# Kernel tuning notes

Hardware: AMD Instinct MI355X
Metric: run time of the kernel (lower is better)

The kernel has to match this reference:

```python
import jax, jax.numpy as jnp
import numpy as np

B, S, D, VOCAB, K = 32, 128, 300, 20000, 8


def setup_inputs() -> dict:
    key = jax.random.key(0)
    ks = jax.random.split(key, 12)
    return {
        "words": jax.random.normal(ks[0], (B, S, D), jnp.float32),
        "lengths": jax.random.randint(ks[1], (B,), S // 2, S + 1),
        "vocab": jax.random.normal(ks[2], (VOCAB, D), jnp.float32) * 0.1,
        "default_embed": jax.random.uniform(ks[3], (D,), jnp.float32),
        "W": jnp.eye(D, dtype=jnp.float32) + 0.01 * jax.random.normal(ks[4], (D, D), jnp.float32),
        "lstm_Wih": jax.random.normal(ks[5], (4 * D, D), jnp.float32) * 0.05,
        "lstm_Whh": jax.random.normal(ks[6], (4 * D, D), jnp.float32) * 0.05,
        "lstm_bih": jnp.zeros((4 * D,), jnp.float32),
        "lstm_bhh": jnp.zeros((4 * D,), jnp.float32),
        "rnn_Wih": jax.random.normal(ks[7], (D, D), jnp.float32) * 0.05,
        "rnn_Whh": jax.random.normal(ks[8], (D, D), jnp.float32) * 0.05,
        "rnn_bih": jnp.zeros((D,), jnp.float32),
        "rnn_bhh": jnp.zeros((D,), jnp.float32),
    }


def _forward(words, lengths, vocab, default_embed, W,
             lstm_Wih, lstm_Whh, lstm_bih, lstm_bhh,
             rnn_Wih, rnn_Whh, rnn_bih, rnn_bhh):
    b, s, d = words.shape
    # --- NormalizeWordsModel (tagger) ---
    C = jnp.concatenate([vocab.T, default_embed[:, None]], axis=1)  # [D, V+1]
    P = jax.nn.softmax(jnp.einsum("bsd,de,ev->bsv", words, W, C), axis=-1)  # [B,S,V+1]
    V = P[..., -1:] * words + jnp.einsum("bsv,vd->bsd", P[..., :-1], vocab)  # [B,S,D]

    # --- LSTM encoder, final hidden at true length (packed-sequence semantics) ---
    valid = (jnp.arange(s)[None, :] < lengths[:, None])  # [B,S]

    def lstm_step(carry, xs):
        h, c = carry
        x_t, v_t = xs  # [B,D], [B]
        gates = x_t @ lstm_Wih.T + lstm_bih + h @ lstm_Whh.T + lstm_bhh  # [B,4D]
        i, f, g, o = jnp.split(gates, 4, axis=-1)
        c_new = jax.nn.sigmoid(f) * c + jax.nn.sigmoid(i) * jnp.tanh(g)
        h_new = jax.nn.sigmoid(o) * jnp.tanh(c_new)
        m = v_t[:, None]
        h = jnp.where(m, h_new, h)
        c = jnp.where(m, c_new, c)
        return (h, c), None

    h0 = jnp.zeros((b, d), V.dtype)
    (q, _), _ = jax.lax.scan(lstm_step, (h0, h0),
                             (jnp.swapaxes(V, 0, 1), valid.T))  # q: [B,D]

    # --- InstructionsDecoder: RNNCell applied K times to the same input q ---
    def rnn_step(h, _):
        h2 = jnp.tanh(q @ rnn_Wih.T + rnn_bih + h @ rnn_Whh.T + rnn_bhh)
        return h2, h2

    _, H = jax.lax.scan(rnn_step, h0, None, length=K)  # [K,B,D]
    H = jnp.swapaxes(H, 0, 1)  # [B,K,D]

    # --- masked softmax attention readout ---
    scores = jnp.einsum("bkd,bsd->bks", H, V)  # [B,K,S]
    scores = jnp.where(valid[:, None, :], scores, -jnp.inf)
    R = jnp.einsum("bks,bsd->bkd", jax.nn.softmax(scores, axis=-1), V)
    return R


def reference(words, lengths, vocab, default_embed, W,
              lstm_Wih, lstm_Whh, lstm_bih, lstm_bhh,
              rnn_Wih, rnn_Whh, rnn_bih, rnn_bhh):
    return _forward(words, lengths, vocab, default_embed, W,
                    lstm_Wih, lstm_Whh, lstm_bih, lstm_bhh,
                    rnn_Wih, rnn_Whh, rnn_bih, rnn_bhh)
```

## Files before the change

kernel.cpp:

```cpp
#include <hip/hip_runtime.h>


typedef unsigned short u16;
typedef unsigned int   u32;
typedef float  f32x4 __attribute__((ext_vector_type(4)));
typedef u32    u32x4 __attribute__((ext_vector_type(4)));
typedef __bf16 bf16x8 __attribute__((ext_vector_type(8)));
typedef _Float16 f16x2 __attribute__((ext_vector_type(2)));
typedef _Float16 f16x8 __attribute__((ext_vector_type(8)));

#define SCOPE_AGENT __HIP_MEMORY_SCOPE_AGENT

__device__ __forceinline__ float bf2f(u16 u) { return __uint_as_float(((u32)u) << 16); }
__device__ __forceinline__ u16 f2bf(float f) {
  u32 x = __float_as_uint(f);
  u32 r = (x + 0x7fffu + ((x >> 16) & 1u)) >> 16;
  return (u16)r;
}
__device__ __forceinline__ float sigm(float x) { return 1.f / (1.f + __expf(-x)); }
__device__ __forceinline__ u16 f2h(float f) {
  union { _Float16 h; u16 u; } cv; cv.h = (_Float16)f; return cv.u;
}
__device__ __forceinline__ float h2f(u16 u) {
  union { _Float16 h; u16 u; } cv; cv.u = u; return (float)cv.h;
}

__device__ __forceinline__ f32x4 shflx4(f32x4 v, int m) {
  f32x4 r;
  r[0] = __shfl_xor(v[0], m, 16);
  r[1] = __shfl_xor(v[1], m, 16);
  r[2] = __shfl_xor(v[2], m, 16);
  r[3] = __shfl_xor(v[3], m, 16);
  return r;
}

__device__ __forceinline__ void conv_seg(const void* src, u16* dst, int n, int is32,
                                         int t0, int stride) {
  if (is32) {
    const float* s = (const float*)src;
    for (int i = t0; i < n; i += stride) dst[i] = f2bf(s[i]);
  } else {
    const u16* s = (const u16*)src;
    for (int i = t0; i < n; i += stride) dst[i] = s[i];
  }
}

__global__ __launch_bounds__(256) void k_ingest(
    const void* words, const void* vocab, const void* de, const void* W,
    const void* lWih, const void* lWhh, const void* lbih, const void* lbhh,
    const void* rWih, const void* rWhh, const void* rbih, const void* rbhh,
    u16* cw, u16* cv, u16* cde, u16* cW, u16* cWih, u16* cWhh, u16* cbih, u16* cbhh,
    u16* crWih, u16* crWhh, u16* crbih, u16* crbhh, u32* flag, u32* seqz, u32* hbz) {
  __shared__ int s_is32;
  int tid = threadIdx.x;
  int vote = 0;
  if (tid < 64) {
    u32 w = ((const u32*)words)[tid];
    int e = (w >> 7) & 0xFF;
    vote = (e >= 100 && e <= 150) ? 1 : 0;
  }
  unsigned long long m = __ballot(vote);
  if (tid == 0) s_is32 = (__popcll(m) < 32) ? 1 : 0;
  __syncthreads();
  int is32 = s_is32;
  if (blockIdx.x == 0 && tid == 0) *flag = (u32)is32;
  int t0 = blockIdx.x * 256 + tid;
  int stride = gridDim.x * 256;
  if (t0 < 256) seqz[t0] = 0;
  if (t0 < 10240) hbz[t0] = 0;
  conv_seg(words, cw, 1228800, is32, t0, stride);
  conv_seg(vocab, cv, 6000000, is32, t0, stride);
  conv_seg(de, cde, 300, is32, t0, stride);
  conv_seg(W, cW, 90000, is32, t0, stride);
  conv_seg(lWih, cWih, 360000, is32, t0, stride);
  conv_seg(lWhh, cWhh, 360000, is32, t0, stride);
  conv_seg(lbih, cbih, 1200, is32, t0, stride);
  conv_seg(lbhh, cbhh, 1200, is32, t0, stride);
  conv_seg(rWih, crWih, 90000, is32, t0, stride);
  conv_seg(rWhh, crWhh, 90000, is32, t0, stride);
  conv_seg(rbih, crbih, 300, is32, t0, stride);
  conv_seg(rbhh, crbhh, 300, is32, t0, stride);
}

__global__ __launch_bounds__(256) void k_transpose_bf(const u16* __restrict__ in,
                                                      u16* __restrict__ out,
                                                      int J, int K) {
  __shared__ u16 t[32][33];
  int j0 = blockIdx.x * 32, k0 = blockIdx.y * 32;
  int lx = threadIdx.x & 31, ly = threadIdx.x >> 5;
  for (int r = ly; r < 32; r += 8) {
    int j = j0 + r, k = k0 + lx;
    t[r][lx] = (j < J && k < K) ? in[(size_t)j * K + k] : (u16)0;
  }
  __syncthreads();
  for (int r = ly; r < 32; r += 8) {
    int k = k0 + r, j = j0 + lx;
    if (k < K && j < J) out[(size_t)k * J + j] = t[lx][r];
  }
}

__global__ __launch_bounds__(256) void k_pack_w4(const u16* __restrict__ Whh,
                                                 u16* __restrict__ pW) {
  int idx = blockIdx.x * 256 + threadIdx.x;
  if (idx >= 16 * 25600) return;
  int bid = idx / 25600, r = idx % 25600;
  int t2 = r >> 9, lane = (r >> 3) & 63, j = r & 7;
  int nt = t2 / 10, kt = t2 % 10;
  int n = nt * 16 + (lane & 15);
  int gate = n / 20, dl = n % 20;
  int d0 = (bid < 15) ? 19 * bid : 285;
  int nd = (bid < 15) ? 19 : 15;
  int k = kt * 32 + ((lane >> 4) * 8) + j;
  u16 out = 0;
  if (dl < nd && k < 300) out = f2h(bf2f(Whh[(size_t)(gate * 300 + d0 + dl) * 300 + k]));
  pW[idx] = out;
}

__global__ __launch_bounds__(256) void k_pack_vocab(const u16* __restrict__ vocab,
                                                    u16* __restrict__ pA,
                                                    u16* __restrict__ pB) {
  __shared__ u16 sv[32][320];
  int ci = blockIdx.x, tid = threadIdx.x;
  for (int idx = tid; idx < 32 * 20; idx += 256) {
    int v = idx / 20, k = 300 + (idx - v * 20);
    sv[v][k] = 0;
  }
  for (int idx = tid; idx < 32 * 300; idx += 256) {
    int v = idx / 300, k = idx - v * 300;
    sv[v][k] = vocab[(size_t)(ci * 32 + v) * 300 + k];
  }
  __syncthreads();
  for (int idx = tid; idx < 10240; idx += 256) {
    int j = idx & 7, lane = (idx >> 3) & 63, t2 = idx >> 9;
    int kk = t2 % 10, h = t2 / 10;
    int v = h * 16 + (lane & 15);
    int k = kk * 32 + ((lane >> 4)) * 8 + j;
    pA[(size_t)ci * 10240 + (size_t)idx] = sv[v][k];
  }
  for (int idx = tid; idx < 9728; idx += 256) {
    int j = idx & 7, lane = (idx >> 3) & 63, nc = idx >> 9;
    int v = (lane >> 4) * 8 + j;
    int n = nc * 16 + (lane & 15);
    pB[(size_t)ci * 9728 + (size_t)idx] = sv[v][n];
  }
}

__global__ __launch_bounds__(256) void k_xw(const u16* __restrict__ words,
                                            const u16* __restrict__ W,
                                            u16* __restrict__ X) {
  __shared__ float As[300][33];
  int n0 = blockIdx.x * 128;
  int r0 = blockIdx.y * 32;
  int tid = threadIdx.x;
  for (int idx = tid; idx < 32 * 300; idx += 256) {
    int r = idx / 300, k = idx - r * 300;
    As[k][r] = bf2f(words[(size_t)(r0 + r) * 300 + k]);
  }
  __syncthreads();
  int j = n0 + (tid & 127);
  int rh = (tid >> 7) * 16;
  float acc[16];
#pragma unroll
  for (int i = 0; i < 16; i++) acc[i] = 0.f;
  if (j < 300) {
    for (int k = 0; k < 300; k++) {
      float bw = bf2f(W[(size_t)k * 300 + j]);
#pragma unroll
      for (int i = 0; i < 16; i++) acc[i] += As[k][rh + i] * bw;
    }
  }
  if (j < 320) {
#pragma unroll
    for (int i = 0; i < 16; i++) {
      float v = (j < 300) ? acc[i] : 0.f;
      X[(size_t)(r0 + rh + i) * 320 + j] = f2bf(v);
    }
  }
}

__global__ __launch_bounds__(512, 2) void k_softmax_v(
    const u16* __restrict__ X, const u16* __restrict__ pA, const u16* __restrict__ pB,
    u16* __restrict__ pAcc, float* __restrict__ pML) {
  __shared__ __align__(16) u16 chunk[19968];
  __shared__ __align__(16) float ptbuf[8 * 576];
  int bid = blockIdx.x;
  int sl = bid & 7, b = bid >> 3;
  int tid = threadIdx.x;
  int w = tid >> 6, lane = tid & 63;
  int quad = lane >> 4, n16 = lane & 15;
  int cs = (sl == 0) ? 0 : 79 + (sl - 1) * 78;
  int nch = (sl == 0) ? 79 : 78;

  int rowA = b * 128 + w * 16 + n16;
  const bf16x8* Xrow = (const bf16x8*)(X + (size_t)rowA * 320);
  bf16x8 afr[10];
#pragma unroll
  for (int kk = 0; kk < 10; kk++) afr[kk] = Xrow[kk * 4 + quad];
// ... 104 lines not shown
  }
#pragma unroll
  for (int nc = 0; nc < 19; nc++)
#pragma unroll
    for (int r = 0; r < 4; r++)
      pAcc[(prow + quad * 4 + r) * 304 + nc * 16 + n16] = f2bf(acc[nc][r]);
}

__global__ __launch_bounds__(320) void k_combine(
    const u16* __restrict__ pAcc, const float* __restrict__ pML,
    const u16* __restrict__ X, const u16* __restrict__ de,
    const u16* __restrict__ words, u16* __restrict__ Vout) {
  __shared__ float red[320];
  __shared__ float fs[8];
  __shared__ float sinv, sw;
  int row = blockIdx.x, tid = threadIdx.x;
  float p = 0.f;
  if (tid < 300) p = bf2f(X[(size_t)row * 320 + tid]) * bf2f(de[tid]);
  red[tid] = p;
  __syncthreads();
  if (tid == 0) {
    float d = 0.f;
    for (int i = 0; i < 300; i++) d += red[i];
    float mv[8], lv[8], ms = -1e30f;
    for (int s = 0; s < 8; s++) {
      mv[s] = pML[((size_t)s * 4096 + row) * 2];
      lv[s] = pML[((size_t)s * 4096 + row) * 2 + 1];
      ms = fmaxf(ms, mv[s]);
    }
    float mf = fmaxf(ms, d);
    float pd = __expf(d - mf);
    float l = pd;
    for (int s = 0; s < 8; s++) {
      float f = __expf(mv[s] - mf);
      fs[s] = f;
      l += lv[s] * f;
    }
    sinv = 1.f / l;
    sw = pd / l;
  }
  __syncthreads();
  float v = 0.f;
  if (tid < 300) {
    float a = 0.f;
#pragma unroll
    for (int s = 0; s < 8; s++)
      a += bf2f(pAcc[((size_t)s * 4096 + row) * 304 + tid]) * fs[s];
    v = a * sinv + sw * bf2f(words[(size_t)row * 300 + tid]);
  }
  Vout[(size_t)row * 320 + tid] = f2bf(v);
}

__global__ __launch_bounds__(256) void k_xg(const u16* __restrict__ Vb,
                                            const u16* __restrict__ WihT,
                                            const u16* __restrict__ bih,
                                            const u16* __restrict__ bhh,
                                            float* __restrict__ xg) {
  __shared__ float As[300][33];
  int n0 = blockIdx.x * 128;
  int r0 = blockIdx.y * 32;
  int tid = threadIdx.x;
  for (int idx = tid; idx < 32 * 300; idx += 256) {
    int r = idx / 300, k = idx - r * 300;
    As[k][r] = bf2f(Vb[(size_t)(r0 + r) * 320 + k]);
  }
  __syncthreads();
  int j = n0 + (tid & 127);
  if (j >= 1200) return;
  int rh = (tid >> 7) * 16;
  float acc[16];
#pragma unroll
  for (int i = 0; i < 16; i++) acc[i] = 0.f;
  for (int k = 0; k < 300; k++) {
    float bw = bf2f(WihT[(size_t)k * 1200 + j]);
#pragma unroll
    for (int i = 0; i < 16; i++) acc[i] += As[k][rh + i] * bw;
  }
  float bias = bf2f(bih[j]) + bf2f(bhh[j]);
#pragma unroll
  for (int i = 0; i < 16; i++)
    xg[(size_t)(r0 + rh + i) * 1200 + j] = acc[i] + bias;
}

__global__ __launch_bounds__(320, 1) void k_lstm2(
    const float* __restrict__ xg, const u16* __restrict__ pW,
    const int* __restrict__ lengths, u16* __restrict__ hb, u32* __restrict__ seq) {
  __shared__ float gl[32][84];
  __shared__ int s_maxlen;
  int bid = blockIdx.x, tid = threadIdx.x;
  int w = tid >> 6, lane = tid & 63;
  int quad = lane >> 4, n16 = lane & 15;
  int d0 = (bid < 15) ? 19 * bid : 285;
  int nd = (bid < 15) ? 19 : 15;
  {
    int lv = (tid < 32) ? lengths[tid] : 0;
    for (int off2 = 1; off2 < 32; off2 <<= 1) {
      int o = __shfl_xor(lv, off2, 64);
      lv = lv > o ? lv : o;
    }
    if (tid == 0) s_maxlen = lv;
  }
  f16x8 bf[10];
  const u32x4* pw4 = (const u32x4*)(pW + (size_t)bid * 25600);
#pragma unroll
  for (int kt = 0; kt < 10; kt++)
    bf[kt] = __builtin_bit_cast(f16x8, pw4[(w * 10 + kt) * 64 + lane]);
  int b0 = tid / 20, dl0 = tid - b0 * 20;
  int b1 = (tid + 320) / 20, dl1 = (tid + 320) - b1 * 20;
  bool a0 = dl0 < nd, a1 = dl1 < nd;
  int len0 = lengths[b0], len1 = lengths[b1];
  int dim0 = d0 + dl0, dim1 = d0 + dl1;
  int sa0 = (((b0 >> 4) * 10 + (dim0 >> 5)) * 64 + ((dim0 >> 3) & 3) * 16 + (b0 & 15)) * 8 + (dim0 & 7);
  int sa1 = (((b1 >> 4) * 10 + (dim1 >> 5)) * 64 + ((dim1 >> 3) & 3) * 16 + (b1 & 15)) * 8 + (dim1 & 7);
  float c0 = 0.f, h0 = 0.f, c1 = 0.f, h1 = 0.f;
  __syncthreads();
  int maxlen = s_maxlen;
  for (int t = 0; t < maxlen; t++) {
    if (tid < 16) {
      while (__hip_atomic_load(&seq[tid * 16], __ATOMIC_ACQUIRE, SCOPE_AGENT) < (u32)t)
        __builtin_amdgcn_s_sleep(2);
    }
    __syncthreads();
    float xv00 = 0.f, xv01 = 0.f, xv02 = 0.f, xv03 = 0.f;
    float xv10 = 0.f, xv11 = 0.f, xv12 = 0.f, xv13 = 0.f;
    const float* xr0 = xg + ((size_t)b0 * 128 + t) * 1200 + dim0;
    const float* xr1 = xg + ((size_t)b1 * 128 + t) * 1200 + dim1;
    if (a0) { xv00 = xr0[0]; xv01 = xr0[300]; xv02 = xr0[600]; xv03 = xr0[900]; }
    if (a1) { xv10 = xr1[0]; xv11 = xr1[300]; xv12 = xr1[600]; xv13 = xr1[900]; }
    const u32x4* hbt = (const u32x4*)hb + (size_t)(t & 1) * 1280;
    u32x4 af[2][10];
#pragma unroll
    for (int mt = 0; mt < 2; mt++)
#pragma unroll
      for (int kt = 0; kt < 10; kt++)
        af[mt][kt] = hbt[(mt * 10 + kt) * 64 + lane];
#pragma unroll
    for (int mt = 0; mt < 2; mt++) {
      f32x4 C;
      C[0] = 0.f; C[1] = 0.f; C[2] = 0.f; C[3] = 0.f;
#pragma unroll
      for (int kt = 0; kt < 10; kt++)
        C = __builtin_amdgcn_mfma_f32_16x16x32_f16(
            __builtin_bit_cast(f16x8, af[mt][kt]), bf[kt], C, 0, 0, 0);
#pragma unroll
      for (int rr = 0; rr < 4; rr++)
        gl[mt * 16 + quad * 4 + rr][w * 16 + n16] = C[rr];
    }
    __syncthreads();
    u16* hbw = hb + (size_t)((t + 1) & 1) * 10240;
    if (a0) {
      float gi = gl[b0][dl0] + xv00, gf = gl[b0][20 + dl0] + xv01;
      float gg = gl[b0][40 + dl0] + xv02, go = gl[b0][60 + dl0] + xv03;
      if (t < len0) {
        c0 = sigm(gf) * c0 + sigm(gi) * tanhf(gg);
        h0 = sigm(go) * tanhf(c0);
      }
      hbw[sa0] = f2h(h0);
    }
    if (a1) {
      float gi = gl[b1][dl1] + xv10, gf = gl[b1][20 + dl1] + xv11;
      float gg = gl[b1][40 + dl1] + xv12, go = gl[b1][60 + dl1] + xv13;
      if (t < len1) {
        c1 = sigm(gf) * c1 + sigm(gi) * tanhf(gg);
        h1 = sigm(go) * tanhf(c1);
      }
      hbw[sa1] = f2h(h1);
    }
    __syncthreads();
    if (tid == 0)
      __hip_atomic_store(&seq[bid * 16], (u32)(t + 1), __ATOMIC_RELEASE, SCOPE_AGENT);
  }
}

__global__ __launch_bounds__(320) void k_rnn(
    const u16* __restrict__ hb, const int* __restrict__ lengths,
    const u16* __restrict__ rWihT, const u16* __restrict__ rWhhT,
    const u16* __restrict__ rbih, const u16* __restrict__ rbhh,
    float* __restrict__ H) {
  __shared__ float qs[304], h2[304], base[304];
  __shared__ int s_maxlen;
  int b = blockIdx.x, tid = threadIdx.x;
  {
    int lv = (tid < 32) ? lengths[tid] : 0;
    for (int off2 = 1; off2 < 32; off2 <<= 1) {
      int o = __shfl_xor(lv, off2, 64);
      lv = lv > o ? lv : o;
    }
    if (tid == 0) s_maxlen = lv;
  }
  __syncthreads();
  int buf = s_maxlen & 1;
  if (tid < 304) {
    float q = 0.f;
    if (tid < 300) {
      int dim = tid;
      int idx = (((b >> 4) * 10 + (dim >> 5)) * 64 + ((dim >> 3) & 3) * 16 + (b & 15)) * 8 + (dim & 7);
      q = h2f(hb[(size_t)buf * 10240 + idx]);
    }
    qs[tid] = q;
    h2[tid] = 0.f;
  }
  __syncthreads();
  if (tid < 300) {
    float a = bf2f(rbih[tid]) + bf2f(rbhh[tid]);
    for (int k = 0; k < 300; k++) a += qs[k] * bf2f(rWihT[(size_t)k * 300 + tid]);
    base[tid] = a;
  }
  __syncthreads();
  for (int s = 0; s < 8; s++) {
    float nv = 0.f;
    if (tid < 300) {
      float a = base[tid];
      for (int k = 0; k < 300; k++) a += h2[k] * bf2f(rWhhT[(size_t)k * 300 + tid]);
      nv = tanhf(a);
    }
    __syncthreads();
    if (tid < 300) {
      h2[tid] = nv;
      H[((size_t)b * 8 + s) * 300 + tid] = nv;
    }
    __syncthreads();
  }
}

__global__ __launch_bounds__(256) void k_attn(const float* __restrict__ H,
                                              const u16* __restrict__ Vb,
                                              const int* __restrict__ lengths,
                                              const u32* __restrict__ flag,
                                              void* __restrict__ dout) {
  __shared__ float Hs[8][304];
  __shared__ float sc[8][128];
  __shared__ float wsum[8];
  int b = blockIdx.x, tid = threadIdx.x;
  int len = lengths[b];
  int is32 = (int)*flag;
  for (int idx = tid; idx < 8 * 300; idx += 256) {
    int k = idx / 300, j = idx - k * 300;
    Hs[k][j] = H[((size_t)b * 8 + k) * 300 + j];
  }
  __syncthreads();
  for (int s = tid; s < len; s += 256) {
    const u16* vr = Vb + (size_t)(b * 128 + s) * 320;
    float a[8];
#pragma unroll
    for (int k = 0; k < 8; k++) a[k] = 0.f;
    for (int j = 0; j < 300; j++) {
      float v = bf2f(vr[j]);
#pragma unroll
      for (int k = 0; k < 8; k++) a[k] += Hs[k][j] * v;
    }
#pragma unroll
    for (int k = 0; k < 8; k++) sc[k][s] = a[k];
  }
  __syncthreads();
  if (tid < 8) {
    float m = -1e30f;
    for (int s = 0; s < len; s++) m = fmaxf(m, sc[tid][s]);
    float l = 0.f;
    for (int s = 0; s < len; s++) { float e = __expf(sc[tid][s] - m); sc[tid][s] = e; l += e; }
    wsum[tid] = 1.f / l;
  }
  __syncthreads();
  int k = tid >> 5, jl = tid & 31;
  for (int j = jl; j < 300; j += 32) {
    float a = 0.f;
    for (int s = 0; s < len; s++) a += sc[k][s] * bf2f(Vb[(size_t)(b * 128 + s) * 320 + j]);
    float val = a * wsum[k];
    size_t o = ((size_t)b * 8 + k) * 300 + j;
    if (is32) ((float*)dout)[o] = val;
    else ((u16*)dout)[o] = f2bf(val);
  }
}

extern "C" void kernel_launch(void* const* d_in, const int* in_sizes, int n_in,
                              void* d_out, int out_size, void* d_ws, size_t ws_size,
                              hipStream_t stream) {
  (void)in_sizes; (void)n_in; (void)out_size; (void)ws_size;
  const void* words = d_in[0];
  const int* lengths = (const int*)d_in[1];
  const void* vocab = d_in[2];
  const void* de = d_in[3];
  const void* W = d_in[4];
  const void* lWih = d_in[5];
  const void* lWhh = d_in[6];
  const void* lbih = d_in[7];
  const void* lbhh = d_in[8];
  const void* rWih = d_in[9];
  const void* rWhh = d_in[10];
  const void* rbih = d_in[11];
  const void* rbhh = d_in[12];

  char* basep = (char*)d_ws;
  size_t off = 0;
  auto take = [&](size_t bytes) -> char* {
    char* p = basep + off;
    off += (bytes + 255) & ~(size_t)255;
    return p;
  };
  u16* cw    = (u16*)take(1228800 * 2);
  u16* cv    = (u16*)take(6000000 * 2);
  u16* cde   = (u16*)take(300 * 2);
  u16* cW    = (u16*)take(90000 * 2);
  u16* cWih  = (u16*)take(360000 * 2);
  u16* cWhh  = (u16*)take(360000 * 2);
  u16* cbih  = (u16*)take(1200 * 2);
  u16* cbhh  = (u16*)take(1200 * 2);
  u16* crWih = (u16*)take(90000 * 2);
  u16* crWhh = (u16*)take(90000 * 2);
  u16* crbih = (u16*)take(300 * 2);
  u16* crbhh = (u16*)take(300 * 2);
  u32* flag  = (u32*)take(256);
  u16*   X     = (u16*)take((size_t)4096 * 320 * 2);
  u16*   Vb    = (u16*)take((size_t)4096 * 320 * 2);
  u16*   WihT  = (u16*)take((size_t)300 * 1200 * 2);
  u16*   pW4   = (u16*)take((size_t)16 * 25600 * 2);
  u16*   rWihT = (u16*)take((size_t)300 * 300 * 2);
  u16*   rWhhT = (u16*)take((size_t)300 * 300 * 2);
  u16*   pAcc  = (u16*)take((size_t)8 * 4096 * 304 * 2);
  float* pML   = (float*)take((size_t)8 * 4096 * 2 * 4);
  float* H     = (float*)take((size_t)32 * 8 * 300 * 4);
  u16*   hb    = (u16*)take((size_t)2 * 10240 * 2);
  u32*   seq   = (u32*)take((size_t)4096 * 4);
  char* ureg = take((size_t)25000192);
  u16*   pA = (u16*)ureg;
  u16*   pB = (u16*)(ureg + (size_t)625 * 10240 * 2);
  float* xg = (float*)ureg;

  k_ingest<<<4096, 256, 0, stream>>>(words, vocab, de, W, lWih, lWhh, lbih, lbhh,
                                     rWih, rWhh, rbih, rbhh,
                                     cw, cv, cde, cW, cWih, cWhh, cbih, cbhh,
                                     crWih, crWhh, crbih, crbhh, flag, seq, (u32*)hb);
  k_transpose_bf<<<dim3(38, 10), 256, 0, stream>>>(cWih, WihT, 1200, 300);
  k_transpose_bf<<<dim3(10, 10), 256, 0, stream>>>(crWih, rWihT, 300, 300);
  k_transpose_bf<<<dim3(10, 10), 256, 0, stream>>>(crWhh, rWhhT, 300, 300);
  k_pack_w4<<<1600, 256, 0, stream>>>(cWhh, pW4);
  k_pack_vocab<<<625, 256, 0, stream>>>(cv, pA, pB);
  k_xw<<<dim3(3, 128), 256, 0, stream>>>(cw, cW, X);
  k_softmax_v<<<256, 512, 0, stream>>>(X, pA, pB, pAcc, pML);
  k_combine<<<4096, 320, 0, stream>>>(pAcc, pML, X, cde, cw, Vb);
  k_xg<<<dim3(10, 128), 256, 0, stream>>>(Vb, WihT, cbih, cbhh, xg);
  k_lstm2<<<16, 320, 0, stream>>>(xg, pW4, lengths, hb, seq);
  k_rnn<<<32, 320, 0, stream>>>(hb, lengths, rWihT, rWhhT, crbih, crbhh, H);
  k_attn<<<32, 256, 0, stream>>>(H, Vb, lengths, flag, d_out);
}
```

Baseline: 1.083 ms.

## Replace cross-block LSTM recurrence with per-batch-half single-block kernel

The LSTM recurrence no longer spreads hidden dimensions over 16 blocks that sync through global atomic flags every timestep. Instead, 2 blocks of 1024 threads each own 16 batch rows and all 300 dims, keep the whole Whh in registers, and exchange h through double-buffered LDS. A new repack kernel reorders the input gate projections so each lane can prefetch its gate quadruple, and gate values are gathered with DPP lane swaps. Sigmoid and tanh use rcp-based fast approximations. This removes the global spin-wait and barrier cost on the serial critical path, but uses only 2 CUs, adds an extra repack pass, and may hurt accuracy through the fast math.

```diff
diff --git a/kernel.cpp b/kernel.cpp
--- a/kernel.cpp
+++ b/kernel.cpp
@@ -9,20 +9,29 @@
 typedef _Float16 f16x2 __attribute__((ext_vector_type(2)));
 typedef _Float16 f16x8 __attribute__((ext_vector_type(8)));
 
-#define SCOPE_AGENT __HIP_MEMORY_SCOPE_AGENT
-
 __device__ __forceinline__ float bf2f(u16 u) { return __uint_as_float(((u32)u) << 16); }
 __device__ __forceinline__ u16 f2bf(float f) {
   u32 x = __float_as_uint(f);
   u32 r = (x + 0x7fffu + ((x >> 16) & 1u)) >> 16;
   return (u16)r;
 }
-__device__ __forceinline__ float sigm(float x) { return 1.f / (1.f + __expf(-x)); }
 __device__ __forceinline__ u16 f2h(float f) {
   union { _Float16 h; u16 u; } cv; cv.h = (_Float16)f; return cv.u;
 }
 __device__ __forceinline__ float h2f(u16 u) {
   union { _Float16 h; u16 u; } cv; cv.u = u; return (float)cv.h;
+}
+__device__ __forceinline__ float sigm_fast(float x) {
+  return __builtin_amdgcn_rcpf(1.f + __expf(-x));
+}
+__device__ __forceinline__ float tanh_fast(float x) {
+  return 1.f - 2.f * __builtin_amdgcn_rcpf(1.f + __expf(2.f * x));
+}
+
+template <int CTRL>
+__device__ __forceinline__ float dppq(float v) {
+  return __uint_as_float(
+      (u32)__builtin_amdgcn_mov_dpp((int)__float_as_uint(v), CTRL, 0xF, 0xF, true));
 }
 
 __device__ __forceinline__ f32x4 shflx4(f32x4 v, int m) {
@@ -50,7 +59,7 @@
     const void* lWih, const void* lWhh, const void* lbih, const void* lbhh,
     const void* rWih, const void* rWhh, const void* rbih, const void* rbhh,
     u16* cw, u16* cv, u16* cde, u16* cW, u16* cWih, u16* cWhh, u16* cbih, u16* cbhh,
-    u16* crWih, u16* crWhh, u16* crbih, u16* crbhh, u32* flag, u32* seqz, u32* hbz) {
+    u16* crWih, u16* crWhh, u16* crbih, u16* crbhh, u32* flag) {
   __shared__ int s_is32;
   int tid = threadIdx.x;
   int vote = 0;
@@ -66,8 +75,6 @@
   if (blockIdx.x == 0 && tid == 0) *flag = (u32)is32;
   int t0 = blockIdx.x * 256 + tid;
   int stride = gridDim.x * 256;
-  if (t0 < 256) seqz[t0] = 0;
-  if (t0 < 10240) hbz[t0] = 0;
   conv_seg(words, cw, 1228800, is32, t0, stride);
   conv_seg(vocab, cv, 6000000, is32, t0, stride);
   conv_seg(de, cde, 300, is32, t0, stride);
@@ -99,20 +106,26 @@
   }
 }
 
-__global__ __launch_bounds__(256) void k_pack_w4(const u16* __restrict__ Whh,
+__global__ __launch_bounds__(256) void k_pack_w5(const u16* __restrict__ Whh,
                                                  u16* __restrict__ pW) {
   int idx = blockIdx.x * 256 + threadIdx.x;
-  if (idx >= 16 * 25600) return;
-  int bid = idx / 25600, r = idx % 25600;
-  int t2 = r >> 9, lane = (r >> 3) & 63, j = r & 7;
-  int nt = t2 / 10, kt = t2 % 10;
-  int n = nt * 16 + (lane & 15);
-  int gate = n / 20, dl = n % 20;
-  int d0 = (bid < 15) ? 19 * bid : 285;
-  int nd = (bid < 15) ? 19 : 15;
-  int k = kt * 32 + ((lane >> 4) * 8) + j;
+  if (idx >= 409600) return;
+  int jj = idx & 7;
+  int lane = (idx >> 3) & 63;
+  int rest = idx >> 9;
+  int kt = rest % 10;
+  int t2 = rest / 10;
+  int j = t2 % 5;
+  int w = t2 / 5;
+  int n16 = lane & 15;
+  int g2 = n16 & 3;
+  int local = j * 16 + n16;
+  int dd = local >> 2;
+  int dim = w * 20 + dd;
+  int k = kt * 32 + ((lane >> 4) * 8) + jj;
   u16 out = 0;
-  if (dl < nd && k < 300) out = f2h(bf2f(Whh[(size_t)(gate * 300 + d0 + dl) * 300 + k]));
+  if (dim < 300 && k < 300)
+    out = f2h(bf2f(Whh[(size_t)(g2 * 300 + dim) * 300 + k]));
   pW[idx] = out;
 }
 
@@ -383,122 +396,136 @@
     xg[(size_t)(r0 + rh + i) * 1200 + j] = acc[i] + bias;
 }
 
-__global__ __launch_bounds__(320, 1) void k_lstm2(
-    const float* __restrict__ xg, const u16* __restrict__ pW,
-    const int* __restrict__ lengths, u16* __restrict__ hb, u32* __restrict__ seq) {
-  __shared__ float gl[32][84];
+__global__ __launch_bounds__(256) void k_repack_xg(const float* __restrict__ xg,
+                                                   float* __restrict__ xgp) {
+  __shared__ float s[16][81];
+  int bid = blockIdx.x;
+  int t = bid & 127, bm = bid >> 7;
+  int tid = threadIdx.x;
+  for (int w = 0; w < 16; w++) {
+    for (int e = tid; e < 1280; e += 256) {
+      int bl = e / 80, local = e - bl * 80;
+      int g2 = local / 20, dd = local - g2 * 20;
+      int dim = w * 20 + dd;
+      float v = 0.f;
+      if (dim < 300)
+        v = xg[((size_t)(bm * 16 + bl) * 128 + t) * 1200 + g2 * 300 + dim];
+      s[bl][dd * 4 + g2] = v;
+    }
+    __syncthreads();
+    size_t ob = ((size_t)(t * 2 + bm) * 1280 + w * 80) * 16;
+    for (int e = tid; e < 1280; e += 256) {
+      int nl = e >> 4, bl = e & 15;
+      xgp[ob + e] = s[bl][nl];
+    }
+    __syncthreads();
+  }
+}
+
+__global__ __launch_bounds__(1024, 1) void k_lstm3(
+    const float* __restrict__ xgp, const u16* __restrict__ pW,
+    const int* __restrict__ lengths, float* __restrict__ qbuf) {
+  __shared__ u16 hs[2][16][328];
   __shared__ int s_maxlen;
-  int bid = blockIdx.x, tid = threadIdx.x;
+  int bm = blockIdx.x, tid = threadIdx.x;
   int w = tid >> 6, lane = tid & 63;
   int quad = lane >> 4, n16 = lane & 15;
-  int d0 = (bid < 15) ? 19 * bid : 285;
-  int nd = (bid < 15) ? 19 : 15;
+  int g = n16 & 3, q4 = n16 >> 2;
+  for (int i = tid; i < 2 * 16 * 328; i += 1024) ((u16*)hs)[i] = 0;
   {
-    int lv = (tid < 32) ? lengths[tid] : 0;
-    for (int off2 = 1; off2 < 32; off2 <<= 1) {
-      int o = __shfl_xor(lv, off2, 64);
+    int lv = (lane < 16) ? lengths[bm * 16 + lane] : 0;
+#pragma unroll
+    for (int off = 1; off < 16; off <<= 1) {
+      int o = __shfl_xor(lv, off, 64);
       lv = lv > o ? lv : o;
     }
     if (tid == 0) s_maxlen = lv;
   }
-  f16x8 bf[10];
-  const u32x4* pw4 = (const u32x4*)(pW + (size_t)bid * 25600);
-#pragma unroll
-  for (int kt = 0; kt < 10; kt++)
-    bf[kt] = __builtin_bit_cast(f16x8, pw4[(w * 10 + kt) * 64 + lane]);
-  int b0 = tid / 20, dl0 = tid - b0 * 20;
-  int b1 = (tid + 320) / 20, dl1 = (tid + 320) - b1 * 20;
-  bool a0 = dl0 < nd, a1 = dl1 < nd;
-  int len0 = lengths[b0], len1 = lengths[b1];
-  int dim0 = d0 + dl0, dim1 = d0 + dl1;
-  int sa0 = (((b0 >> 4) * 10 + (dim0 >> 5)) * 64 + ((dim0 >> 3) & 3) * 16 + (b0 & 15)) * 8 + (dim0 & 7);
-  int sa1 = (((b1 >> 4) * 10 + (dim1 >> 5)) * 64 + ((dim1 >> 3) & 3) * 16 + (b1 & 15)) * 8 + (dim1 & 7);
-  float c0 = 0.f, h0 = 0.f, c1 = 0.f, h1 = 0.f;
+  f16x8 bf[5][10];
+  const u32x4* pw4 = (const u32x4*)pW;
+#pragma unroll
+  for (int j = 0; j < 5; j++)
+#pragma unroll
+    for (int kt = 0; kt < 10; kt++)
+      bf[j][kt] = __builtin_bit_cast(f16x8, pw4[((w * 5 + j) * 10 + kt) * 64 + lane]);
+  int b = quad * 4 + g;
+  int len_b = lengths[bm * 16 + b];
+  float c[5], h[5];
+#pragma unroll
+  for (int j = 0; j < 5; j++) { c[j] = 0.f; h[j] = 0.f; }
+  const f32x4* xp0 = (const f32x4*)xgp + ((size_t)bm * 1280 + w * 80 + n16) * 4 + quad;
+  f32x4 xv[5];
+#pragma unroll
+  for (int j = 0; j < 5; j++) xv[j] = xp0[j * 64];
   __syncthreads();
   int maxlen = s_maxlen;
   for (int t = 0; t < maxlen; t++) {
-    if (tid < 16) {
-      while (__hip_atomic_load(&seq[tid * 16], __ATOMIC_ACQUIRE, SCOPE_AGENT) < (u32)t)
-        __builtin_amdgcn_s_sleep(2);
-    }
-    __syncthreads();
-    float xv00 = 0.f, xv01 = 0.f, xv02 = 0.f, xv03 = 0.f;
-    float xv10 = 0.f, xv11 = 0.f, xv12 = 0.f, xv13 = 0.f;
-    const float* xr0 = xg + ((size_t)b0 * 128 + t) * 1200 + dim0;
-    const float* xr1 = xg + ((size_t)b1 * 128 + t) * 1200 + dim1;
-    if (a0) { xv00 = xr0[0]; xv01 = xr0[300]; xv02 = xr0[600]; xv03 = xr0[900]; }
-    if (a1) { xv10 = xr1[0]; xv11 = xr1[300]; xv12 = xr1[600]; xv13 = xr1[900]; }
-    const u32x4* hbt = (const u32x4*)hb + (size_t)(t & 1) * 1280;
-    u32x4 af[2][10];
-#pragma unroll
-    for (int mt = 0; mt < 2; mt++)
-#pragma unroll
-      for (int kt = 0; kt < 10; kt++)
-        af[mt][kt] = hbt[(mt * 10 + kt) * 64 + lane];
-#pragma unroll
-    for (int mt = 0; mt < 2; mt++) {
-      f32x4 C;
-      C[0] = 0.f; C[1] = 0.f; C[2] = 0.f; C[3] = 0.f;
-#pragma unroll
-      for (int kt = 0; kt < 10; kt++)
-        C = __builtin_amdgcn_mfma_f32_16x16x32_f16(
-            __builtin_bit_cast(f16x8, af[mt][kt]), bf[kt], C, 0, 0, 0);
-#pragma unroll
-      for (int rr = 0; rr < 4; rr++)
-        gl[mt * 16 + quad * 4 + rr][w * 16 + n16] = C[rr];
-    }
-    __syncthreads();
-    u16* hbw = hb + (size_t)((t + 1) & 1) * 10240;
-    if (a0) {
-      float gi = gl[b0][dl0] + xv00, gf = gl[b0][20 + dl0] + xv01;
-      float gg = gl[b0][40 + dl0] + xv02, go = gl[b0][60 + dl0] + xv03;
-      if (t < len0) {
-        c0 = sigm(gf) * c0 + sigm(gi) * tanhf(gg);
-        h0 = sigm(go) * tanhf(c0);
-      }
-      hbw[sa0] = f2h(h0);
-    }
-    if (a1) {
-      float gi = gl[b1][dl1] + xv10, gf = gl[b1][20 + dl1] + xv11;
-      float gg = gl[b1][40 + dl1] + xv12, go = gl[b1][60 + dl1] + xv13;
-      if (t < len1) {
-        c1 = sigm(gf) * c1 + sigm(gi) * tanhf(gg);
-        h1 = sigm(go) * tanhf(c1);
-      }
-      hbw[sa1] = f2h(h1);
-    }
-    __syncthreads();
-    if (tid == 0)
-      __hip_atomic_store(&seq[bid * 16], (u32)(t + 1), __ATOMIC_RELEASE, SCOPE_AGENT);
+    f32x4 acc[5];
+#pragma unroll
+    for (int j = 0; j < 5; j++) acc[j] = xv[j];
+    if (t + 1 < maxlen) {
+      const f32x4* xp = xp0 + (size_t)(t + 1) * 10240;
+#pragma unroll
+      for (int j = 0; j < 5; j++) xv[j] = xp[j * 64];
+    }
+    const u16* hr = &hs[t & 1][0][0];
+    u32x4 af[10];
+#pragma unroll
+    for (int kt = 0; kt < 10; kt++)
+      af[kt] = *(const u32x4*)(hr + n16 * 328 + kt * 32 + quad * 8);
+#pragma unroll
+    for (int kt = 0; kt < 10; kt++) {
+      f16x8 a = __builtin_bit_cast(f16x8, af[kt]);
+#pragma unroll
+      for (int j = 0; j < 5; j++)
+        acc[j] = __builtin_amdgcn_mfma_f32_16x16x32_f16(a, bf[j][kt], acc[j], 0, 0, 0);
+    }
+    u16* hw = (u16*)&hs[(t + 1) & 1][0][0];
+    bool upd = (t < len_b);
+#pragma unroll
+    for (int j = 0; j < 5; j++) {
+      float v0 = acc[j][0], v1 = acc[j][1], v2 = acc[j][2], v3 = acc[j][3];
+      float x0 = dppq<0xB1>(v0), x1 = dppq<0xB1>(v1);
+      float x2 = dppq<0xB1>(v2), x3 = dppq<0xB1>(v3);
+      bool o1 = (g & 1);
+      float m0 = o1 ? x1 : v0;
+      float m1 = o1 ? v1 : x0;
+      float m2 = o1 ? x3 : v2;
+      float m3 = o1 ? v3 : x2;
+      float y0 = dppq<0x4E>(m0), y1 = dppq<0x4E>(m1);
+      float y2 = dppq<0x4E>(m2), y3 = dppq<0x4E>(m3);
+      bool o2 = (g & 2);
+      float F0 = o2 ? y2 : m0;
+      float F1 = o2 ? y3 : m1;
+      float F2 = o2 ? m2 : y0;
+      float F3 = o2 ? m3 : y1;
+      float ii = sigm_fast(F0), ff = sigm_fast(F1);
+      float gg = tanh_fast(F2), oo = sigm_fast(F3);
+      float cn = ff * c[j] + ii * gg;
+      float hn = oo * tanh_fast(cn);
+      c[j] = upd ? cn : c[j];
+      h[j] = upd ? hn : h[j];
+      int dim = w * 20 + j * 4 + q4;
+      if (dim < 300) hw[b * 328 + dim] = f2h(h[j]);
+    }
+    __syncthreads();
+  }
+#pragma unroll
+  for (int j = 0; j < 5; j++) {
+    int dim = w * 20 + j * 4 + q4;
+    if (dim < 300) qbuf[(size_t)(bm * 16 + b) * 304 + dim] = h[j];
   }
 }
 
 __global__ __launch_bounds__(320) void k_rnn(
-    const u16* __restrict__ hb, const int* __restrict__ lengths,
+    const float* __restrict__ qbuf,
     const u16* __restrict__ rWihT, const u16* __restrict__ rWhhT,
     const u16* __restrict__ rbih, const u16* __restrict__ rbhh,
     float* __restrict__ H) {
   __shared__ float qs[304], h2[304], base[304];
-  __shared__ int s_maxlen;
   int b = blockIdx.x, tid = threadIdx.x;
-  {
-    int lv = (tid < 32) ? lengths[tid] : 0;
-    for (int off2 = 1; off2 < 32; off2 <<= 1) {
-      int o = __shfl_xor(lv, off2, 64);
-      lv = lv > o ? lv : o;
-    }
-    if (tid == 0) s_maxlen = lv;
-  }
-  __syncthreads();
-  int buf = s_maxlen & 1;
   if (tid < 304) {
-    float q = 0.f;
-    if (tid < 300) {
-      int dim = tid;
-      int idx = (((b >> 4) * 10 + (dim >> 5)) * 64 + ((dim >> 3) & 3) * 16 + (b & 15)) * 8 + (dim & 7);
-      q = h2f(hb[(size_t)buf * 10240 + idx]);
-    }
-    qs[tid] = q;
+    qs[tid] = (tid < 300) ? qbuf[(size_t)b * 304 + tid] : 0.f;
     h2[tid] = 0.f;
   }
   __syncthreads();
@@ -614,14 +641,15 @@
   u16*   X     = (u16*)take((size_t)4096 * 320 * 2);
   u16*   Vb    = (u16*)take((size_t)4096 * 320 * 2);
   u16*   WihT  = (u16*)take((size_t)300 * 1200 * 2);
-  u16*   pW4   = (u16*)take((size_t)16 * 25600 * 2);
+  u16*   pW5   = (u16*)take((size_t)409600 * 2);
   u16*   rWihT = (u16*)take((size_t)300 * 300 * 2);
   u16*   rWhhT = (u16*)take((size_t)300 * 300 * 2);
-  u16*   pAcc  = (u16*)take((size_t)8 * 4096 * 304 * 2);
+  char* uacc = take((size_t)20971520);
+  u16*   pAcc = (u16*)uacc;
+  float* xgp  = (float*)uacc;
   float* pML   = (float*)take((size_t)8 * 4096 * 2 * 4);
   float* H     = (float*)take((size_t)32 * 8 * 300 * 4);
-  u16*   hb    = (u16*)take((size_t)2 * 10240 * 2);
-  u32*   seq   = (u32*)take((size_t)4096 * 4);
+  float* qbuf  = (float*)take((size_t)32 * 304 * 4);
   char* ureg = take((size_t)25000192);
   u16*   pA = (u16*)ureg;
   u16*   pB = (u16*)(ureg + (size_t)625 * 10240 * 2);
@@ -630,17 +658,18 @@
   k_ingest<<<4096, 256, 0, stream>>>(words, vocab, de, W, lWih, lWhh, lbih, lbhh,
                                      rWih, rWhh, rbih, rbhh,
                                      cw, cv, cde, cW, cWih, cWhh, cbih, cbhh,
-                                     crWih, crWhh, crbih, crbhh, flag, seq, (u32*)hb);
+                                     crWih, crWhh, crbih, crbhh, flag);
   k_transpose_bf<<<dim3(38, 10), 256, 0, stream>>>(cWih, WihT, 1200, 300);
   k_transpose_bf<<<dim3(10, 10), 256, 0, stream>>>(crWih, rWihT, 300, 300);
   k_transpose_bf<<<dim3(10, 10), 256, 0, stream>>>(crWhh, rWhhT, 300, 300);
-  k_pack_w4<<<1600, 256, 0, stream>>>(cWhh, pW4);
+  k_pack_w5<<<1600, 256, 0, stream>>>(cWhh, pW5);
   k_pack_vocab<<<625, 256, 0, stream>>>(cv, pA, pB);
   k_xw<<<dim3(3, 128), 256, 0, stream>>>(cw, cW, X);
   k_softmax_v<<<256, 512, 0, stream>>>(X, pA, pB, pAcc, pML);
   k_combine<<<4096, 320, 0, stream>>>(pAcc, pML, X, cde, cw, Vb);
   k_xg<<<dim3(10, 128), 256, 0, stream>>>(Vb, WihT, cbih, cbhh, xg);
-  k_lstm2<<<16, 320, 0, stream>>>(xg, pW4, lengths, hb, seq);
-  k_rnn<<<32, 320, 0, stream>>>(hb, lengths, rWihT, rWhhT, crbih, crbhh, H);
+  k_repack_xg<<<256, 256, 0, stream>>>(xg, xgp);
+  k_lstm3<<<2, 1024, 0, stream>>>(xgp, pW5, lengths, qbuf);
+  k_rnn<<<32, 320, 0, stream>>>(qbuf, rWihT, rWhhT, crbih, crbhh, H);
   k_attn<<<32, 256, 0, stream>>>(H, Vb, lengths, flag, d_out);
 }
```

Result: slower. 2.995 ms (+176.6%).

## Split LSTM recurrence over 8 larger blocks with LDS weights and relaxed flags

Applied to the files above, without the earlier changes.

The persistent LSTM recurrence now runs on 8 blocks of 640 threads instead of 16 blocks of 320, so each step waits on half as many cross-block flags. Each block now covers 38 hidden dimensions, and its recurrent-weight slice is staged in LDS. The hidden-state exchange uses relaxed atomic loads and stores with a shorter sleep, and sigmoid and tanh use fast reciprocal-based approximations. The final hidden state is written to a float buffer for the RNN kernel, which removes the fp16 re-read. Tradeoffs: each block does more work per step, the relaxed ordering leans on the release/acquire flag pattern for correctness, and the fast transcendentals are less precise.

```diff
diff --git a/kernel.cpp b/kernel.cpp
--- a/kernel.cpp
+++ b/kernel.cpp
@@ -6,7 +6,6 @@
 typedef float  f32x4 __attribute__((ext_vector_type(4)));
 typedef u32    u32x4 __attribute__((ext_vector_type(4)));
 typedef __bf16 bf16x8 __attribute__((ext_vector_type(8)));
-typedef _Float16 f16x2 __attribute__((ext_vector_type(2)));
 typedef _Float16 f16x8 __attribute__((ext_vector_type(8)));
 
 #define SCOPE_AGENT __HIP_MEMORY_SCOPE_AGENT
@@ -17,12 +16,17 @@
   u32 r = (x + 0x7fffu + ((x >> 16) & 1u)) >> 16;
   return (u16)r;
 }
-__device__ __forceinline__ float sigm(float x) { return 1.f / (1.f + __expf(-x)); }
 __device__ __forceinline__ u16 f2h(float f) {
   union { _Float16 h; u16 u; } cv; cv.h = (_Float16)f; return cv.u;
 }
 __device__ __forceinline__ float h2f(u16 u) {
   union { _Float16 h; u16 u; } cv; cv.u = u; return (float)cv.h;
+}
+__device__ __forceinline__ float sigm_fast(float x) {
+  return __builtin_amdgcn_rcpf(1.f + __expf(-x));
+}
+__device__ __forceinline__ float tanh_fast(float x) {
+  return 1.f - 2.f * __builtin_amdgcn_rcpf(1.f + __expf(2.f * x));
 }
 
 __device__ __forceinline__ f32x4 shflx4(f32x4 v, int m) {
@@ -99,20 +103,25 @@
   }
 }
 
-__global__ __launch_bounds__(256) void k_pack_w4(const u16* __restrict__ Whh,
+__global__ __launch_bounds__(256) void k_pack_w8(const u16* __restrict__ Whh,
                                                  u16* __restrict__ pW) {
   int idx = blockIdx.x * 256 + threadIdx.x;
-  if (idx >= 16 * 25600) return;
-  int bid = idx / 25600, r = idx % 25600;
-  int t2 = r >> 9, lane = (r >> 3) & 63, j = r & 7;
-  int nt = t2 / 10, kt = t2 % 10;
-  int n = nt * 16 + (lane & 15);
-  int gate = n / 20, dl = n % 20;
-  int d0 = (bid < 15) ? 19 * bid : 285;
-  int nd = (bid < 15) ? 19 : 15;
-  int k = kt * 32 + ((lane >> 4) * 8) + j;
+  if (idx >= 409600) return;
+  int bid = idx / 51200;
+  int r = idx - bid * 51200;
+  int j = r & 7;
+  int lane = (r >> 3) & 63;
+  int t2 = r >> 9;
+  int kt = t2 % 10, w = t2 / 10;
+  int n16 = lane & 15, quad = lane >> 4;
+  int n = w * 16 + n16;
+  int gate = n / 40, dl = n - gate * 40;
+  int nd = (bid < 7) ? 38 : 34;
+  int dim = 38 * bid + dl;
+  int k = kt * 32 + quad * 8 + j;
   u16 out = 0;
-  if (dl < nd && k < 300) out = f2h(bf2f(Whh[(size_t)(gate * 300 + d0 + dl) * 300 + k]));
+  if (dl < nd && k < 300)
+    out = f2h(bf2f(Whh[(size_t)(gate * 300 + dim) * 300 + k]));
   pW[idx] = out;
 }
 
@@ -383,122 +392,131 @@
     xg[(size_t)(r0 + rh + i) * 1200 + j] = acc[i] + bias;
 }
 
-__global__ __launch_bounds__(320, 1) void k_lstm2(
+__global__ __launch_bounds__(640, 1) void k_lstm5(
     const float* __restrict__ xg, const u16* __restrict__ pW,
-    const int* __restrict__ lengths, u16* __restrict__ hb, u32* __restrict__ seq) {
-  __shared__ float gl[32][84];
+    const int* __restrict__ lengths, u32* __restrict__ hb,
+    u32* __restrict__ seq, float* __restrict__ qbuf) {
+  __shared__ __align__(16) u16 wlds[51200];
+  __shared__ float gl[32][164];
   __shared__ int s_maxlen;
   int bid = blockIdx.x, tid = threadIdx.x;
   int w = tid >> 6, lane = tid & 63;
   int quad = lane >> 4, n16 = lane & 15;
-  int d0 = (bid < 15) ? 19 * bid : 285;
-  int nd = (bid < 15) ? 19 : 15;
+  int nd = (bid < 7) ? 38 : 34;
+  {
+    const u32x4* src = (const u32x4*)(pW + (size_t)bid * 51200);
+    u32x4* dst = (u32x4*)wlds;
+#pragma unroll
+    for (int i = 0; i < 10; i++) dst[tid + i * 640] = src[tid + i * 640];
+  }
   {
     int lv = (tid < 32) ? lengths[tid] : 0;
-    for (int off2 = 1; off2 < 32; off2 <<= 1) {
-      int o = __shfl_xor(lv, off2, 64);
+#pragma unroll
+    for (int off = 1; off < 32; off <<= 1) {
+      int o = __shfl_xor(lv, off, 64);
       lv = lv > o ? lv : o;
     }
     if (tid == 0) s_maxlen = lv;
   }
-  f16x8 bf[10];
-  const u32x4* pw4 = (const u32x4*)(pW + (size_t)bid * 25600);
-#pragma unroll
-  for (int kt = 0; kt < 10; kt++)
-    bf[kt] = __builtin_bit_cast(f16x8, pw4[(w * 10 + kt) * 64 + lane]);
-  int b0 = tid / 20, dl0 = tid - b0 * 20;
-  int b1 = (tid + 320) / 20, dl1 = (tid + 320) - b1 * 20;
-  bool a0 = dl0 < nd, a1 = dl1 < nd;
+  int b0 = tid / 40, dl = tid - b0 * 40;
+  int b1 = b0 + 16;
+  bool act = dl < nd;
+  int dim = 38 * bid + dl;
   int len0 = lengths[b0], len1 = lengths[b1];
-  int dim0 = d0 + dl0, dim1 = d0 + dl1;
-  int sa0 = (((b0 >> 4) * 10 + (dim0 >> 5)) * 64 + ((dim0 >> 3) & 3) * 16 + (b0 & 15)) * 8 + (dim0 & 7);
-  int sa1 = (((b1 >> 4) * 10 + (dim1 >> 5)) * 64 + ((dim1 >> 3) & 3) * 16 + (b1 & 15)) * 8 + (dim1 & 7);
+  int p = (dim >> 1) & 3;
+  int chq = ((dim >> 3) & 3) * 16;
+  int ch0 = ((0 * 10 + (dim >> 5)) * 64 + chq + (b0 & 15));
+  int ch1 = ((1 * 10 + (dim >> 5)) * 64 + chq + (b1 & 15));
+  int so0 = (p * 1280 + ch0) * 2 + (dim & 1);
+  int so1 = (p * 1280 + ch1) * 2 + (dim & 1);
+  u16* hb16 = (u16*)hb;
   float c0 = 0.f, h0 = 0.f, c1 = 0.f, h1 = 0.f;
+  u32* myf = seq + (size_t)bid * 16;
   __syncthreads();
   int maxlen = s_maxlen;
   for (int t = 0; t < maxlen; t++) {
-    if (tid < 16) {
-      while (__hip_atomic_load(&seq[tid * 16], __ATOMIC_ACQUIRE, SCOPE_AGENT) < (u32)t)
-        __builtin_amdgcn_s_sleep(2);
+    if (tid < 8) {
+      while (__hip_atomic_load(&seq[tid * 16], __ATOMIC_RELAXED, SCOPE_AGENT) < (u32)t)
+        __builtin_amdgcn_s_sleep(1);
     }
     __syncthreads();
     float xv00 = 0.f, xv01 = 0.f, xv02 = 0.f, xv03 = 0.f;
     float xv10 = 0.f, xv11 = 0.f, xv12 = 0.f, xv13 = 0.f;
-    const float* xr0 = xg + ((size_t)b0 * 128 + t) * 1200 + dim0;
-    const float* xr1 = xg + ((size_t)b1 * 128 + t) * 1200 + dim1;
-    if (a0) { xv00 = xr0[0]; xv01 = xr0[300]; xv02 = xr0[600]; xv03 = xr0[900]; }
-    if (a1) { xv10 = xr1[0]; xv11 = xr1[300]; xv12 = xr1[600]; xv13 = xr1[900]; }
-    const u32x4* hbt = (const u32x4*)hb + (size_t)(t & 1) * 1280;
+    if (act) {
+      const float* xr0 = xg + ((size_t)b0 * 128 + t) * 1200 + dim;
+      const float* xr1 = xg + ((size_t)b1 * 128 + t) * 1200 + dim;
+      xv00 = xr0[0]; xv01 = xr0[300]; xv02 = xr0[600]; xv03 = xr0[900];
+      xv10 = xr1[0]; xv11 = xr1[300]; xv12 = xr1[600]; xv13 = xr1[900];
+    }
+    const u32* hbt = hb + (size_t)(t & 1) * 5120;
     u32x4 af[2][10];
 #pragma unroll
     for (int mt = 0; mt < 2; mt++)
 #pragma unroll
       for (int kt = 0; kt < 10; kt++)
-        af[mt][kt] = hbt[(mt * 10 + kt) * 64 + lane];
-#pragma unroll
-    for (int mt = 0; mt < 2; mt++) {
-      f32x4 C;
-      C[0] = 0.f; C[1] = 0.f; C[2] = 0.f; C[3] = 0.f;
-#pragma unroll
-      for (int kt = 0; kt < 10; kt++)
-        C = __builtin_amdgcn_mfma_f32_16x16x32_f16(
-            __builtin_bit_cast(f16x8, af[mt][kt]), bf[kt], C, 0, 0, 0);
-#pragma unroll
-      for (int rr = 0; rr < 4; rr++)
-        gl[mt * 16 + quad * 4 + rr][w * 16 + n16] = C[rr];
-    }
-    __syncthreads();
-    u16* hbw = hb + (size_t)((t + 1) & 1) * 10240;
-    if (a0) {
-      float gi = gl[b0][dl0] + xv00, gf = gl[b0][20 + dl0] + xv01;
-      float gg = gl[b0][40 + dl0] + xv02, go = gl[b0][60 + dl0] + xv03;
-      if (t < len0) {
-        c0 = sigm(gf) * c0 + sigm(gi) * tanhf(gg);
-        h0 = sigm(go) * tanhf(c0);
+#pragma unroll
+        for (int pp = 0; pp < 4; pp++)
+          af[mt][kt][pp] = __hip_atomic_load(
+              hbt + pp * 1280 + (mt * 10 + kt) * 64 + lane,
+              __ATOMIC_RELAXED, SCOPE_AGENT);
+    const u32x4* wl = (const u32x4*)wlds;
+    f32x4 C0, C1;
+    C0[0] = 0.f; C0[1] = 0.f; C0[2] = 0.f; C0[3] = 0.f;
+    C1[0] = 0.f; C1[1] = 0.f; C1[2] = 0.f; C1[3] = 0.f;
+#pragma unroll
+    for (int kt = 0; kt < 10; kt++) {
+      f16x8 bfr = __builtin_bit_cast(f16x8, wl[(w * 10 + kt) * 64 + lane]);
+      C0 = __builtin_amdgcn_mfma_f32_16x16x32_f16(
+          __builtin_bit_cast(f16x8, af[0][kt]), bfr, C0, 0, 0, 0);
+      C1 = __builtin_amdgcn_mfma_f32_16x16x32_f16(
+          __builtin_bit_cast(f16x8, af[1][kt]), bfr, C1, 0, 0, 0);
+    }
+#pragma unroll
+    for (int rr = 0; rr < 4; rr++) {
+      gl[quad * 4 + rr][w * 16 + n16] = C0[rr];
+      gl[16 + quad * 4 + rr][w * 16 + n16] = C1[rr];
+    }
+    __syncthreads();
+    int bufo = ((t + 1) & 1) * 10240;
+    if (act) {
+      {
+        float gi = gl[b0][dl] + xv00, gf = gl[b0][40 + dl] + xv01;
+        float gg = gl[b0][80 + dl] + xv02, go = gl[b0][120 + dl] + xv03;
+        if (t < len0) {
+          c0 = sigm_fast(gf) * c0 + sigm_fast(gi) * tanh_fast(gg);
+          h0 = sigm_fast(go) * tanh_fast(c0);
+        }
+        __hip_atomic_store(hb16 + bufo + so0, f2h(h0), __ATOMIC_RELAXED, SCOPE_AGENT);
       }
-      hbw[sa0] = f2h(h0);
-    }
-    if (a1) {
-      float gi = gl[b1][dl1] + xv10, gf = gl[b1][20 + dl1] + xv11;
-      float gg = gl[b1][40 + dl1] + xv12, go = gl[b1][60 + dl1] + xv13;
-      if (t < len1) {
-        c1 = sigm(gf) * c1 + sigm(gi) * tanhf(gg);
-        h1 = sigm(go) * tanhf(c1);
+      {
+        float gi = gl[b1][dl] + xv10, gf = gl[b1][40 + dl] + xv11;
+        float gg = gl[b1][80 + dl] + xv12, go = gl[b1][120 + dl] + xv13;
+        if (t < len1) {
+          c1 = sigm_fast(gf) * c1 + sigm_fast(gi) * tanh_fast(gg);
+          h1 = sigm_fast(go) * tanh_fast(c1);
+        }
+        __hip_atomic_store(hb16 + bufo + so1, f2h(h1), __ATOMIC_RELAXED, SCOPE_AGENT);
       }
-      hbw[sa1] = f2h(h1);
     }
     __syncthreads();
     if (tid == 0)
-      __hip_atomic_store(&seq[bid * 16], (u32)(t + 1), __ATOMIC_RELEASE, SCOPE_AGENT);
+      __hip_atomic_store(myf, (u32)(t + 1), __ATOMIC_RELEASE, SCOPE_AGENT);
+  }
+  if (act) {
+    qbuf[(size_t)b0 * 304 + dim] = h0;
+    qbuf[(size_t)b1 * 304 + dim] = h1;
   }
 }
 
 __global__ __launch_bounds__(320) void k_rnn(
-    const u16* __restrict__ hb, const int* __restrict__ lengths,
+    const float* __restrict__ qbuf,
     const u16* __restrict__ rWihT, const u16* __restrict__ rWhhT,
     const u16* __restrict__ rbih, const u16* __restrict__ rbhh,
     float* __restrict__ H) {
   __shared__ float qs[304], h2[304], base[304];
-  __shared__ int s_maxlen;
   int b = blockIdx.x, tid = threadIdx.x;
-  {
-    int lv = (tid < 32) ? lengths[tid] : 0;
-    for (int off2 = 1; off2 < 32; off2 <<= 1) {
-      int o = __shfl_xor(lv, off2, 64);
-      lv = lv > o ? lv : o;
-    }
-    if (tid == 0) s_maxlen = lv;
-  }
-  __syncthreads();
-  int buf = s_maxlen & 1;
   if (tid < 304) {
-    float q = 0.f;
-    if (tid < 300) {
-      int dim = tid;
-      int idx = (((b >> 4) * 10 + (dim >> 5)) * 64 + ((dim >> 3) & 3) * 16 + (b & 15)) * 8 + (dim & 7);
-      q = h2f(hb[(size_t)buf * 10240 + idx]);
-    }
-    qs[tid] = q;
+    qs[tid] = (tid < 300) ? qbuf[(size_t)b * 304 + tid] : 0.f;
     h2[tid] = 0.f;
   }
   __syncthreads();
@@ -614,14 +632,15 @@
   u16*   X     = (u16*)take((size_t)4096 * 320 * 2);
   u16*   Vb    = (u16*)take((size_t)4096 * 320 * 2);
   u16*   WihT  = (u16*)take((size_t)300 * 1200 * 2);
-  u16*   pW4   = (u16*)take((size_t)16 * 25600 * 2);
+  u16*   pW8   = (u16*)take((size_t)409600 * 2);
   u16*   rWihT = (u16*)take((size_t)300 * 300 * 2);
   u16*   rWhhT = (u16*)take((size_t)300 * 300 * 2);
   u16*   pAcc  = (u16*)take((size_t)8 * 4096 * 304 * 2);
   float* pML   = (float*)take((size_t)8 * 4096 * 2 * 4);
   float* H     = (float*)take((size_t)32 * 8 * 300 * 4);
-  u16*   hb    = (u16*)take((size_t)2 * 10240 * 2);
-  u32*   seq   = (u32*)take((size_t)4096 * 4);
+  float* qbuf  = (float*)take((size_t)32 * 304 * 4);
+  u32*   hbg   = (u32*)take((size_t)10240 * 4);
+  u32*   seq   = (u32*)take((size_t)1024);
   char* ureg = take((size_t)25000192);
   u16*   pA = (u16*)ureg;
   u16*   pB = (u16*)(ureg + (size_t)625 * 10240 * 2);
@@ -630,17 +649,17 @@
   k_ingest<<<4096, 256, 0, stream>>>(words, vocab, de, W, lWih, lWhh, lbih, lbhh,
                                      rWih, rWhh, rbih, rbhh,
                                      cw, cv, cde, cW, cWih, cWhh, cbih, cbhh,
-                                     crWih, crWhh, crbih, crbhh, flag, seq, (u32*)hb);
+                                     crWih, crWhh, crbih, crbhh, flag, seq, hbg);
   k_transpose_bf<<<dim3(38, 10), 256, 0, stream>>>(cWih, WihT, 1200, 300);
   k_transpose_bf<<<dim3(10, 10), 256, 0, stream>>>(crWih, rWihT, 300, 300);
   k_transpose_bf<<<dim3(10, 10), 256, 0, stream>>>(crWhh, rWhhT, 300, 300);
-  k_pack_w4<<<1600, 256, 0, stream>>>(cWhh, pW4);
+  k_pack_w8<<<1600, 256, 0, stream>>>(cWhh, pW8);
   k_pack_vocab<<<625, 256, 0, stream>>>(cv, pA, pB);
   k_xw<<<dim3(3, 128), 256, 0, stream>>>(cw, cW, X);
   k_softmax_v<<<256, 512, 0, stream>>>(X, pA, pB, pAcc, pML);
   k_combine<<<4096, 320, 0, stream>>>(pAcc, pML, X, cde, cw, Vb);
   k_xg<<<dim3(10, 128), 256, 0, stream>>>(Vb, WihT, cbih, cbhh, xg);
-  k_lstm2<<<16, 320, 0, stream>>>(xg, pW4, lengths, hb, seq);
-  k_rnn<<<32, 320, 0, stream>>>(hb, lengths, rWihT, rWhhT, crbih, crbhh, H);
+  k_lstm5<<<8, 640, 0, stream>>>(xg, pW8, lengths, hbg, seq, qbuf);
+  k_rnn<<<32, 320, 0, stream>>>(qbuf, rWihT, rWhhT, crbih, crbhh, H);
   k_attn<<<32, 256, 0, stream>>>(H, Vb, lengths, flag, d_out);
 }
```

Result: slower. 1.127 ms (+4.1%).
